# Optimization experiments

Hardware: AMD Instinct MI355X
Metric: run time of the kernel (lower is better)

The kernel has to match this reference:

```python
import jax, jax.numpy as jnp
import numpy as np

LEAK = 0.01  # torch F.leaky_relu default slope


def _conv1d(x, W, b):
    # x: [B, Cin, L], W: [Cout, Cin, K] -> [B, Cout, L-K+1]
    y = jax.lax.conv_general_dilated(x, W, window_strides=(1,), padding='VALID',
                                     dimension_numbers=('NCH', 'OIH', 'NCH'))
    return y + b[None, :, None]


def _maxpool3(x):
    # MaxPool1d(kernel=3, stride=3, padding=1); torch pads with -inf
    return jax.lax.reduce_window(x, -jnp.inf, jax.lax.max,
                                 (1, 1, 3), (1, 1, 3),
                                 ((0, 0), (0, 0), (1, 1)))


def _lrelu(x):
    return jnp.where(x >= 0, x, LEAK * x)


def _lstm_layer(x, Wih, Whh, b):
    # x: [B, T, D]; Wih: [4H, D]; Whh: [4H, H]; b: [4H]  (torch gate order i,f,g,o)
    B = x.shape[0]
    H = Whh.shape[1]

    def step(carry, xt):
        h, c = carry
        gates = xt @ Wih.T + h @ Whh.T + b  # [B, 4H]
        i, f, g, o = jnp.split(gates, 4, axis=-1)
        c = jax.nn.sigmoid(f) * c + jax.nn.sigmoid(i) * jnp.tanh(g)
        h = jax.nn.sigmoid(o) * jnp.tanh(c)
        return (h, c), h

    init = (jnp.zeros((B, H), x.dtype), jnp.zeros((B, H), x.dtype))
    _, ys = jax.lax.scan(step, init, jnp.swapaxes(x, 0, 1))
    return jnp.swapaxes(ys, 0, 1)  # [B, T, H]


def _lstm3(x, Wih_s, Whh_s, b_s):
    # 3-layer LSTM (dropout=0 in eval); return h_n[-1] + h_n[-2]
    h_last = []
    for l in range(3):
        x = _lstm_layer(x, Wih_s[l], Whh_s[l], b_s[l])
        h_last.append(x[:, -1])
    return h_last[-1] + h_last[-2]


def _forward(data_in, W1, b1, W2, b2, W3, b3,
             fWih, fWhh, fb, tWih, tWhh, tb,
             L1W, L1b, L2W, L2b, L3W, L3b, L4W, L4b):
    T, F, L, P = data_in.shape
    x = data_in.reshape(T * F, L, P).swapaxes(1, 2)  # [B, 3, L]
    x = _maxpool3(_lrelu(_conv1d(x, W1, b1)))  # [B, 10, 170]
    x = _maxpool3(_lrelu(_conv1d(x, W2, b2)))  # [B, 5, 56]
    x = _maxpool3(_lrelu(_conv1d(x, W3, b3)))  # [B, 10, 18]
    x = x.swapaxes(1, 2)                       # [B, 18, 10] packet vectors
    fv = _lstm3(x, fWih, fWhh, fb)             # [B, 10] flow vectors
    fv = fv.reshape(T, F, -1)                  # [T, F, 10]
    tv = _lstm3(fv, tWih, tWhh, tb)            # [T, 10] trace vectors
    h = _lrelu(tv @ L1W.T + L1b)
    h = _lrelu(h @ L2W.T + L2b)
    h = _lrelu(h @ L3W.T + L3b)
    return h @ L4W.T + L4b                     # [T, 7]


def setup_inputs() -> dict:
    key = jax.random.key(0)
    ks = iter(jax.random.split(key, 32))
    n = lambda shape: jax.random.normal(next(ks), shape, dtype=jnp.float32)
    return {
        'data_in': n((64, 64, 512, 3)),
        'W1': n((10, 3, 5)), 'b1': n((10,)),
        'W2': n((5, 10, 5)), 'b2': n((5,)),
        'W3': n((10, 5, 5)), 'b3': n((10,)),
        'fWih': n((3, 40, 10)), 'fWhh': n((3, 40, 10)), 'fb': n((3, 40)),
        'tWih': n((3, 40, 10)), 'tWhh': n((3, 40, 10)), 'tb': n((3, 40)),
        'L1W': n((128, 10)), 'L1b': n((128,)),
        'L2W': n((256, 128)), 'L2b': n((256,)),
        'L3W': n((64, 256)), 'L3b': n((64,)),
        'L4W': n((7, 64)), 'L4b': n((7,)),
    }


def reference(data_in, W1, b1, W2, b2, W3, b3,
              fWih, fWhh, fb, tWih, tWhh, tb,
              L1W, L1b, L2W, L2b, L3W, L3b, L4W, L4b):
    return _forward(data_in, W1, b1, W2, b2, W3, b3,
                    fWih, fWhh, fb, tWih, tWhh, tb,
                    L1W, L1b, L2W, L2b, L3W, L3b, L4W, L4b)
```

## Files before the change

### kernel.cpp

```cpp
#include <hip/hip_runtime.h>
#include <math.h>

#define LEAK 0.01f

__device__ __forceinline__ float lrelu(float x) { return fmaxf(x, LEAK * x); }
__device__ __forceinline__ float fast_rcp(float x) { return __builtin_amdgcn_rcpf(x); }
__device__ __forceinline__ float sigmoid_f(float x) {
    return fast_rcp(1.0f + exp2f(-1.44269504f * x));
}
__device__ __forceinline__ float tanh_f(float x) {
    return 2.0f * fast_rcp(1.0f + exp2f(-2.88539008f * x)) - 1.0f;
}

#define L1C 508
#define L1P 170
#define L2C 166
#define L2P 56
#define L3C 52
#define L3P 18
#define TT 18

__global__ __launch_bounds__(256) void conv_kernel(
    const float* __restrict__ in,
    const float* __restrict__ W1, const float* __restrict__ b1,
    const float* __restrict__ W2, const float* __restrict__ b2,
    const float* __restrict__ W3, const float* __restrict__ b3,
    float* __restrict__ xseq)
{
    __shared__ __align__(16) float xsraw[24 + 1536 + 24];
    __shared__ __align__(16) float y1raw[16 + L1P * 10 + 32];
    __shared__ __align__(16) float y2raw[8 + L2P * 5 + 24];
    float* xs = xsraw + 24;
    float* y1 = y1raw + 16;
    float* y2 = y2raw + 8;

    const int tid = threadIdx.x;
    const int b = blockIdx.x;

    {
        const float4* src = (const float4*)(in + (size_t)b * 1536);
        float4* dst4 = (float4*)xs;
        for (int i = tid; i < 384; i += 256) dst4[i] = src[i];
    }
    __syncthreads();

    {
        const int co = tid % 10;
        const int ob = tid / 10;
        float w[15];
        #pragma unroll
        for (int q = 0; q < 15; ++q) w[q] = W1[co * 15 + q];
        const float bias = b1[co];
        if (tid < 250) {
            for (int r = 0; r < 7; ++r) {
                int o = ob + 25 * r;
                if (o < L1P) {
                    int t0 = 3 * o - 1;
                    float a0 = bias, a1 = bias, a2 = bias;
                    #pragma unroll
                    for (int p = 0; p < 3; ++p) {
                        float yv[7];
                        #pragma unroll
                        for (int m = 0; m < 7; ++m) yv[m] = xs[3 * (t0 + m) + p];
                        #pragma unroll
                        for (int k = 0; k < 5; ++k) {
                            float wv = w[p * 5 + k];
                            a0 = fmaf(wv, yv[k], a0);
                            a1 = fmaf(wv, yv[k + 1], a1);
                            a2 = fmaf(wv, yv[k + 2], a2);
                        }
                    }
                    float best = -3.0e38f;
                    if (t0 >= 0)        best = fmaxf(best, lrelu(a0));
                    best = fmaxf(best, lrelu(a1));
                    if (t0 + 2 < L1C)   best = fmaxf(best, lrelu(a2));
                    y1[o * 10 + co] = best;
                }
            }
        }
    }
    __syncthreads();

    {
        const int co = tid % 5;
        const int ob = tid / 5;
        float w[50];
        #pragma unroll
        for (int q = 0; q < 50; ++q) w[q] = W2[co * 50 + q];
        const float bias = b2[co];
        if (tid < 255) {
            for (int r = 0; r < 2; ++r) {
                int o = ob + 51 * r;
                if (o < L2P) {
                    int t0 = 3 * o - 1;
                    float a0 = bias, a1 = bias, a2 = bias;
                    #pragma unroll
                    for (int ci = 0; ci < 10; ++ci) {
                        float yv[7];
                        #pragma unroll
                        for (int m = 0; m < 7; ++m) yv[m] = y1[(t0 + m) * 10 + ci];
                        #pragma unroll
                        for (int k = 0; k < 5; ++k) {
                            float wv = w[ci * 5 + k];
                            a0 = fmaf(wv, yv[k], a0);
                            a1 = fmaf(wv, yv[k + 1], a1);
                            a2 = fmaf(wv, yv[k + 2], a2);
                        }
                    }
                    float best = -3.0e38f;
                    if (t0 >= 0)        best = fmaxf(best, lrelu(a0));
                    best = fmaxf(best, lrelu(a1));
                    if (t0 + 2 < L2C)   best = fmaxf(best, lrelu(a2));
                    y2[o * 5 + co] = best;
                }
            }
        }
    }
    __syncthreads();

    {
        const int co = tid % 10;
        const int o = tid / 10;
        if (o < L3P) {
            float w[25];
            #pragma unroll
            for (int q = 0; q < 25; ++q) w[q] = W3[co * 25 + q];
            const float bias = b3[co];
            int t0 = 3 * o - 1;
            float a0 = bias, a1 = bias, a2 = bias;
            #pragma unroll
            for (int ci = 0; ci < 5; ++ci) {
                float yv[7];
                #pragma unroll
                for (int m = 0; m < 7; ++m) yv[m] = y2[(t0 + m) * 5 + ci];
                #pragma unroll
                for (int k = 0; k < 5; ++k) {
                    float wv = w[ci * 5 + k];
                    a0 = fmaf(wv, yv[k], a0);
                    a1 = fmaf(wv, yv[k + 1], a1);
                    a2 = fmaf(wv, yv[k + 2], a2);
                }
            }
            float best = -3.0e38f;
            if (t0 >= 0)        best = fmaxf(best, lrelu(a0));
            best = fmaxf(best, lrelu(a1));
            if (t0 + 2 < L3C)   best = fmaxf(best, lrelu(a2));
            xseq[(size_t)b * 180 + o * 10 + co] = best;
        }
    }
}

__global__ __launch_bounds__(256) void flow_lstm_kernel(
    const float* __restrict__ xseq,
    const float* __restrict__ fWih, const float* __restrict__ fWhh,
    const float* __restrict__ fb,
    float* __restrict__ fv)
{
    __shared__ __align__(16) float sbuf[3][16 * 18 * 10];
    const int tid = threadIdx.x;
    const int blk = blockIdx.x;

    {
        const float* src = xseq + (size_t)blk * 2880;
        for (int i = tid; i < 2880; i += 256) sbuf[0][i] = src[i];
    }
    __syncthreads();

    const int el = tid >> 4;
    const int j = tid & 15;
    const int jj = (j < 10) ? j : 0;
    const int base = el * 180;

    float fv_acc = 0.0f;

    for (int l = 0; l < 3; ++l) {
        const float* Wi = fWih + l * 400;
        const float* Wh = fWhh + l * 400;
        const float* bb = fb + l * 40;
        float wi0[10], wi1[10], wi2[10], wi3[10];
        float wh0[10], wh1[10], wh2[10], wh3[10];
        #pragma unroll
        for (int k = 0; k < 10; ++k) {
            wi0[k] = Wi[jj * 10 + k];
            wi1[k] = Wi[(10 + jj) * 10 + k];
            wi2[k] = Wi[(20 + jj) * 10 + k];
            wi3[k] = Wi[(30 + jj) * 10 + k];
            wh0[k] = Wh[jj * 10 + k];
            wh1[k] = Wh[(10 + jj) * 10 + k];
            wh2[k] = Wh[(20 + jj) * 10 + k];
            wh3[k] = Wh[(30 + jj) * 10 + k];
        }
        const float bi = bb[jj], bf = bb[10 + jj], bg = bb[20 + jj], bo = bb[30 + jj];

        const float* inb = sbuf[l];
        float* outb = sbuf[(l + 1) % 3];
        float c = 0.0f;
        float hj = 0.0f;

        for (int t = 0; t < TT; ++t) {
            float x[10], h[10];
            const float* xp = inb + base + t * 10;
            #pragma unroll
            for (int k = 0; k < 5; ++k) {
                float2 v = ((const float2*)xp)[k];
                x[2 * k] = v.x; x[2 * k + 1] = v.y;
            }
            if (t > 0) {
                const float* hp = outb + base + (t - 1) * 10;
                #pragma unroll
                for (int k = 0; k < 5; ++k) {
                    float2 v = ((const float2*)hp)[k];
                    h[2 * k] = v.x; h[2 * k + 1] = v.y;
                }
            } else {
                #pragma unroll
                for (int k = 0; k < 10; ++k) h[k] = 0.0f;
            }
            float gi = bi, gf = bf, gg = bg, go = bo;
            #pragma unroll
            for (int k = 0; k < 10; ++k) {
                gi = fmaf(wi0[k], x[k], gi); gi = fmaf(wh0[k], h[k], gi);
                gf = fmaf(wi1[k], x[k], gf); gf = fmaf(wh1[k], h[k], gf);
                gg = fmaf(wi2[k], x[k], gg); gg = fmaf(wh2[k], h[k], gg);
                go = fmaf(wi3[k], x[k], go); go = fmaf(wh3[k], h[k], go);
            }
            const float ai = sigmoid_f(gi), af = sigmoid_f(gf);
            const float ag = tanh_f(gg),    ao = sigmoid_f(go);
            c = af * c + ai * ag;
            hj = ao * tanh_f(c);
            if (j < 10) outb[base + t * 10 + j] = hj;
            __asm__ __volatile__("" ::: "memory");
        }
        if (l >= 1) fv_acc += hj;
    }
    if (j < 10) fv[(size_t)(blk * 16 + el) * 10 + j] = fv_acc;
}

__global__ __launch_bounds__(64) void trace_mlp_kernel(
    const float* __restrict__ fv,
    const float* __restrict__ tWih, const float* __restrict__ tWhh,
    const float* __restrict__ tb,
    const float* __restrict__ L1W, const float* __restrict__ L1b,
    const float* __restrict__ L2W, const float* __restrict__ L2b,
    const float* __restrict__ L3W, const float* __restrict__ L3b,
    const float* __restrict__ L4W, const float* __restrict__ L4b,
    float* __restrict__ out)
{
    __shared__ __align__(16) float xrow[640];
    __shared__ __align__(16) float m1[128];
    __shared__ __align__(16) float m2b[256];
    __shared__ __align__(16) float m3[64];

    const int lane = threadIdx.x;
    const int ti = blockIdx.x;

    for (int i = lane; i < 640; i += 64) xrow[i] = fv[(size_t)ti * 640 + i];
    __asm__ __volatile__("" ::: "memory");

    const int gt = lane / 10;
    const bool isg = (gt == 2);
    const float m2g = isg ? 2.0f : 1.0f;
    const float am = isg ? 2.0f : 1.0f;
    const float ab = isg ? -1.0f : 0.0f;

    const int r = (lane < 40) ? lane : 0;
    float wi0[10], wh0[10], wi1[10], wh1[10], wi2[10], wh2[10];
    #pragma unroll
    for (int k = 0; k < 10; ++k) {
        wi0[k] = tWih[r * 10 + k];
        wh0[k] = tWhh[r * 10 + k];
        wi1[k] = tWih[400 + r * 10 + k];
        wh1[k] = tWhh[400 + r * 10 + k];
        wi2[k] = tWih[800 + r * 10 + k];
        wh2[k] = tWhh[800 + r * 10 + k];
    }
    const float bs0 = tb[r], bs1 = tb[40 + r], bs2 = tb[80 + r];

    float hb0[10], hb1[10], hb2[10];
    #pragma unroll
    for (int k = 0; k < 10; ++k) { hb0[k] = 0.0f; hb1[k] = 0.0f; hb2[k] = 0.0f; }
    float c0 = 0.0f, c1 = 0.0f, c2 = 0.0f;

    for (int tick = 0; tick < 66; ++tick) {
        float xn[10];
        if (tick < 64) {
            const float* xp = xrow + tick * 10;
            #pragma unroll
            for (int k = 0; k < 5; ++k) {
                float2 v = ((const float2*)xp)[k];
                xn[2 * k] = v.x; xn[2 * k + 1] = v.y;
            }
        }
        if (tick >= 2) {
            float g = bs2;
            #pragma unroll
            for (int k = 0; k < 10; ++k) {
                g = fmaf(wi2[k], hb1[k], g);
                g = fmaf(wh2[k], hb2[k], g);
            }
            float a = am * sigmoid_f(m2g * g) + ab;
            float af = __shfl(a, lane + 10);
            float ag = __shfl(a, lane + 20);
            float ao = __shfl(a, lane + 30);
            c2 = af * c2 + a * ag;
            float h = ao * tanh_f(c2);
            #pragma unroll
            for (int k = 0; k < 10; ++k) hb2[k] = __shfl(h, k);
        }
        if (tick >= 1 && tick < 65) {
            float g = bs1;
            #pragma unroll
            for (int k = 0; k < 10; ++k) {
                g = fmaf(wi1[k], hb0[k], g);
                g = fmaf(wh1[k], hb1[k], g);
            }
            float a = am * sigmoid_f(m2g * g) + ab;
            float af = __shfl(a, lane + 10);
            float ag = __shfl(a, lane + 20);
            float ao = __shfl(a, lane + 30);
            c1 = af * c1 + a * ag;
            float h = ao * tanh_f(c1);
            #pragma unroll
            for (int k = 0; k < 10; ++k) hb1[k] = __shfl(h, k);
        }
        if (tick < 64) {
            float g = bs0;
            #pragma unroll
            for (int k = 0; k < 10; ++k) {
                g = fmaf(wi0[k], xn[k], g);
                g = fmaf(wh0[k], hb0[k], g);
            }
            float a = am * sigmoid_f(m2g * g) + ab;
            float af = __shfl(a, lane + 10);
            float ag = __shfl(a, lane + 20);
            float ao = __shfl(a, lane + 30);
            c0 = af * c0 + a * ag;
            float h = ao * tanh_f(c0);
            #pragma unroll
            for (int k = 0; k < 10; ++k) hb0[k] = __shfl(h, k);
        }
    }

    float tv[10];
    #pragma unroll
    for (int k = 0; k < 10; ++k) tv[k] = hb1[k] + hb2[k];

    {
        float a0 = L1b[lane], a1 = L1b[lane + 64];
        #pragma unroll
        for (int k = 0; k < 10; ++k) {
            a0 = fmaf(L1W[lane * 10 + k], tv[k], a0);
            a1 = fmaf(L1W[(lane + 64) * 10 + k], tv[k], a1);
        }
        m1[lane] = lrelu(a0);
        m1[lane + 64] = lrelu(a1);
    }
    __asm__ __volatile__("" ::: "memory");
    {
        float acc[4];
        #pragma unroll
        for (int q = 0; q < 4; ++q) acc[q] = L2b[lane + 64 * q];
        for (int k = 0; k < 128; ++k) {
            float hv = m1[k];
            #pragma unroll
            for (int q = 0; q < 4; ++q)
                acc[q] = fmaf(L2W[(size_t)(lane + 64 * q) * 128 + k], hv, acc[q]);
        }
        #pragma unroll
        for (int q = 0; q < 4; ++q) m2b[lane + 64 * q] = lrelu(acc[q]);
    }
    __asm__ __volatile__("" ::: "memory");
    {
        float acc = L3b[lane];
        for (int k = 0; k < 256; ++k)
            acc = fmaf(L3W[(size_t)lane * 256 + k], m2b[k], acc);
        m3[lane] = lrelu(acc);
    }
    __asm__ __volatile__("" ::: "memory");
    if (lane < 7) {
        float acc = L4b[lane];
        #pragma unroll
        for (int k = 0; k < 64; ++k)
            acc = fmaf(L4W[lane * 64 + k], m3[k], acc);
        out[ti * 7 + lane] = acc;
    }
}

extern "C" void kernel_launch(void* const* d_in, const int* in_sizes, int n_in,
                              void* d_out, int out_size, void* d_ws, size_t ws_size,
                              hipStream_t stream)
{
    const float* data_in = (const float*)d_in[0];
    const float* W1 = (const float*)d_in[1];
    const float* b1 = (const float*)d_in[2];
    const float* W2 = (const float*)d_in[3];
    const float* b2 = (const float*)d_in[4];
    const float* W3 = (const float*)d_in[5];
    const float* b3 = (const float*)d_in[6];
    const float* fWih = (const float*)d_in[7];
    const float* fWhh = (const float*)d_in[8];
    const float* fb = (const float*)d_in[9];
    const float* tWih = (const float*)d_in[10];
    const float* tWhh = (const float*)d_in[11];
    const float* tb = (const float*)d_in[12];
    const float* L1W = (const float*)d_in[13];
    const float* L1b = (const float*)d_in[14];
    const float* L2W = (const float*)d_in[15];
    const float* L2b = (const float*)d_in[16];
    const float* L3W = (const float*)d_in[17];
    const float* L3b = (const float*)d_in[18];
    const float* L4W = (const float*)d_in[19];
    const float* L4b = (const float*)d_in[20];

    float* xseq = (float*)d_ws;
    float* fv = xseq + 4096 * 180;
    float* outp = (float*)d_out;

    conv_kernel<<<4096, 256, 0, stream>>>(data_in, W1, b1, W2, b2, W3, b3, xseq);
    flow_lstm_kernel<<<256, 256, 0, stream>>>(xseq, fWih, fWhh, fb, fv);
    trace_mlp_kernel<<<64, 64, 0, stream>>>(fv, tWih, tWhh, tb,
                                            L1W, L1b, L2W, L2b, L3W, L3b,
                                            L4W, L4b, outp);
}
```

Before: 207.5 us.

## Use packed v2f math, sliding conv windows, shuffle-based LSTM hidden broadcast

Conv layer 1 now gives each thread 7 contiguous outputs and slides a register window instead of reloading inputs. Conv layers 2 and 3 use packed two-wide float vectors, and the y2 row stride is padded to 6. The flow LSTM broadcasts the hidden state with wave shuffles instead of reading it back from shared memory, prefetches the next input and uses packed dot products. The trace LSTM is peeled into explicit prologue and epilogue ticks, and the MLP tail uses float4 loads. Together these target FMA issue count and LDS traffic, at the cost of more register pressure and reordered floating-point summation.

```diff
diff --git a/kernel.cpp b/kernel.cpp
--- a/kernel.cpp
+++ b/kernel.cpp
@@ -2,6 +2,8 @@
 #include <math.h>
 
 #define LEAK 0.01f
+
+typedef float v2f __attribute__((ext_vector_type(2)));
 
 __device__ __forceinline__ float lrelu(float x) { return fmaxf(x, LEAK * x); }
 __device__ __forceinline__ float fast_rcp(float x) { return __builtin_amdgcn_rcpf(x); }
@@ -10,6 +12,15 @@
 }
 __device__ __forceinline__ float tanh_f(float x) {
     return 2.0f * fast_rcp(1.0f + exp2f(-2.88539008f * x)) - 1.0f;
+}
+
+__device__ __forceinline__ float dot10(const v2f w[5], const float h[10]) {
+    v2f acc = w[0] * (v2f){h[0], h[1]};
+    acc += w[1] * (v2f){h[2], h[3]};
+    acc += w[2] * (v2f){h[4], h[5]};
+    acc += w[3] * (v2f){h[6], h[7]};
+    acc += w[4] * (v2f){h[8], h[9]};
+    return acc.x + acc.y;
 }
 
 #define L1C 508
@@ -29,7 +40,7 @@
 {
     __shared__ __align__(16) float xsraw[24 + 1536 + 24];
     __shared__ __align__(16) float y1raw[16 + L1P * 10 + 32];
-    __shared__ __align__(16) float y2raw[8 + L2P * 5 + 24];
+    __shared__ __align__(16) float y2raw[8 + L2P * 6 + 24];
     float* xs = xsraw + 24;
     float* y1 = y1raw + 16;
     float* y2 = y2raw + 8;
@@ -47,35 +58,44 @@
     {
         const int co = tid % 10;
         const int ob = tid / 10;
-        float w[15];
-        #pragma unroll
-        for (int q = 0; q < 15; ++q) w[q] = W1[co * 15 + q];
-        const float bias = b1[co];
         if (tid < 250) {
+            float w[15];
+            #pragma unroll
+            for (int q = 0; q < 15; ++q) w[q] = W1[co * 15 + q];
+            const float bias = b1[co];
+            const int o0 = ob * 7;
+            int sb = 3 * o0 - 1;
+            float win[21];
+            #pragma unroll
+            for (int q = 0; q < 21; ++q) win[q] = xs[3 * sb + q];
+            #pragma unroll
             for (int r = 0; r < 7; ++r) {
-                int o = ob + 25 * r;
+                const int o = o0 + r;
                 if (o < L1P) {
-                    int t0 = 3 * o - 1;
                     float a0 = bias, a1 = bias, a2 = bias;
                     #pragma unroll
                     for (int p = 0; p < 3; ++p) {
-                        float yv[7];
-                        #pragma unroll
-                        for (int m = 0; m < 7; ++m) yv[m] = xs[3 * (t0 + m) + p];
                         #pragma unroll
                         for (int k = 0; k < 5; ++k) {
-                            float wv = w[p * 5 + k];
-                            a0 = fmaf(wv, yv[k], a0);
-                            a1 = fmaf(wv, yv[k + 1], a1);
-                            a2 = fmaf(wv, yv[k + 2], a2);
+                            const float wv = w[p * 5 + k];
+                            a0 = fmaf(wv, win[3 * k + p], a0);
+                            a1 = fmaf(wv, win[3 * (k + 1) + p], a1);
+                            a2 = fmaf(wv, win[3 * (k + 2) + p], a2);
                         }
                     }
                     float best = -3.0e38f;
-                    if (t0 >= 0)        best = fmaxf(best, lrelu(a0));
+                    if (sb >= 0)        best = fmaxf(best, lrelu(a0));
                     best = fmaxf(best, lrelu(a1));
-                    if (t0 + 2 < L1C)   best = fmaxf(best, lrelu(a2));
+                    if (sb + 2 < L1C)   best = fmaxf(best, lrelu(a2));
                     y1[o * 10 + co] = best;
                 }
+                if (r < 6 && o + 1 < L1P) {
+                    #pragma unroll
+                    for (int q = 0; q < 12; ++q) win[q] = win[q + 9];
+                    #pragma unroll
+                    for (int q = 0; q < 9; ++q) win[12 + q] = xs[3 * sb + 21 + q];
+                    sb += 3;
+                }
             }
         }
     }
@@ -84,34 +104,45 @@
     {
         const int co = tid % 5;
         const int ob = tid / 5;
-        float w[50];
-        #pragma unroll
-        for (int q = 0; q < 50; ++q) w[q] = W2[co * 50 + q];
+        v2f wv2[25];
+        #pragma unroll
+        for (int c2 = 0; c2 < 5; ++c2)
+            #pragma unroll
+            for (int k = 0; k < 5; ++k)
+                wv2[c2 * 5 + k] = (v2f){W2[co * 50 + (2 * c2) * 5 + k],
+                                        W2[co * 50 + (2 * c2 + 1) * 5 + k]};
         const float bias = b2[co];
         if (tid < 255) {
             for (int r = 0; r < 2; ++r) {
-                int o = ob + 51 * r;
+                const int o = ob + 51 * r;
                 if (o < L2P) {
-                    int t0 = 3 * o - 1;
-                    float a0 = bias, a1 = bias, a2 = bias;
+                    const int t0 = 3 * o - 1;
+                    v2f rows[7][5];
                     #pragma unroll
-                    for (int ci = 0; ci < 10; ++ci) {
-                        float yv[7];
+                    for (int m = 0; m < 7; ++m) {
+                        const v2f* pr = (const v2f*)(y1 + (t0 + m) * 10);
                         #pragma unroll
-                        for (int m = 0; m < 7; ++m) yv[m] = y1[(t0 + m) * 10 + ci];
+                        for (int c2 = 0; c2 < 5; ++c2) rows[m][c2] = pr[c2];
+                    }
+                    v2f v0 = {0.f, 0.f}, v1 = {0.f, 0.f}, v2 = {0.f, 0.f};
+                    #pragma unroll
+                    for (int c2 = 0; c2 < 5; ++c2) {
                         #pragma unroll
                         for (int k = 0; k < 5; ++k) {
-                            float wv = w[ci * 5 + k];
-                            a0 = fmaf(wv, yv[k], a0);
-                            a1 = fmaf(wv, yv[k + 1], a1);
-                            a2 = fmaf(wv, yv[k + 2], a2);
+                            const v2f wv = wv2[c2 * 5 + k];
+                            v0 += wv * rows[k][c2];
+                            v1 += wv * rows[k + 1][c2];
+                            v2 += wv * rows[k + 2][c2];
                         }
                     }
+                    const float a0 = bias + v0.x + v0.y;
+                    const float a1 = bias + v1.x + v1.y;
+                    const float a2 = bias + v2.x + v2.y;
                     float best = -3.0e38f;
                     if (t0 >= 0)        best = fmaxf(best, lrelu(a0));
                     best = fmaxf(best, lrelu(a1));
                     if (t0 + 2 < L2C)   best = fmaxf(best, lrelu(a2));
-                    y2[o * 5 + co] = best;
+                    y2[o * 6 + co] = best;
                 }
             }
         }
@@ -122,25 +153,48 @@
         const int co = tid % 10;
         const int o = tid / 10;
         if (o < L3P) {
-            float w[25];
-            #pragma unroll
-            for (int q = 0; q < 25; ++q) w[q] = W3[co * 25 + q];
+            v2f wv3[10];
+            float ws3[5];
+            #pragma unroll
+            for (int c2 = 0; c2 < 2; ++c2)
+                #pragma unroll
+                for (int k = 0; k < 5; ++k)
+                    wv3[c2 * 5 + k] = (v2f){W3[co * 25 + (2 * c2) * 5 + k],
+                                            W3[co * 25 + (2 * c2 + 1) * 5 + k]};
+            #pragma unroll
+            for (int k = 0; k < 5; ++k) ws3[k] = W3[co * 25 + 20 + k];
             const float bias = b3[co];
-            int t0 = 3 * o - 1;
-            float a0 = bias, a1 = bias, a2 = bias;
-            #pragma unroll
-            for (int ci = 0; ci < 5; ++ci) {
-                float yv[7];
-                #pragma unroll
-                for (int m = 0; m < 7; ++m) yv[m] = y2[(t0 + m) * 5 + ci];
+            const int t0 = 3 * o - 1;
+            v2f ra[7][2];
+            float rc[7];
+            #pragma unroll
+            for (int m = 0; m < 7; ++m) {
+                const float* base = y2 + (t0 + m) * 6;
+                ra[m][0] = ((const v2f*)base)[0];
+                ra[m][1] = ((const v2f*)base)[1];
+                rc[m] = base[4];
+            }
+            v2f v0 = {0.f, 0.f}, v1 = {0.f, 0.f}, v2 = {0.f, 0.f};
+            float s0 = 0.f, s1 = 0.f, s2 = 0.f;
+            #pragma unroll
+            for (int c2 = 0; c2 < 2; ++c2) {
                 #pragma unroll
                 for (int k = 0; k < 5; ++k) {
-                    float wv = w[ci * 5 + k];
-                    a0 = fmaf(wv, yv[k], a0);
-                    a1 = fmaf(wv, yv[k + 1], a1);
-                    a2 = fmaf(wv, yv[k + 2], a2);
+                    const v2f wv = wv3[c2 * 5 + k];
+                    v0 += wv * ra[k][c2];
+                    v1 += wv * ra[k + 1][c2];
+                    v2 += wv * ra[k + 2][c2];
                 }
             }
+            #pragma unroll
+            for (int k = 0; k < 5; ++k) {
+                s0 = fmaf(ws3[k], rc[k], s0);
+                s1 = fmaf(ws3[k], rc[k + 1], s1);
+                s2 = fmaf(ws3[k], rc[k + 2], s2);
+            }
+            const float a0 = bias + s0 + v0.x + v0.y;
+            const float a1 = bias + s1 + v1.x + v1.y;
+            const float a2 = bias + s2 + v2.x + v2.y;
             float best = -3.0e38f;
             if (t0 >= 0)        best = fmaxf(best, lrelu(a0));
             best = fmaxf(best, lrelu(a1));
@@ -170,6 +224,8 @@
     const int j = tid & 15;
     const int jj = (j < 10) ? j : 0;
     const int base = el * 180;
+    const int lane = tid & 63;
+    const int gbase = lane & 48;
 
     float fv_acc = 0.0f;
 
@@ -177,61 +233,54 @@
         const float* Wi = fWih + l * 400;
         const float* Wh = fWhh + l * 400;
         const float* bb = fb + l * 40;
-        float wi0[10], wi1[10], wi2[10], wi3[10];
-        float wh0[10], wh1[10], wh2[10], wh3[10];
-        #pragma unroll
-        for (int k = 0; k < 10; ++k) {
-            wi0[k] = Wi[jj * 10 + k];
-            wi1[k] = Wi[(10 + jj) * 10 + k];
-            wi2[k] = Wi[(20 + jj) * 10 + k];
-            wi3[k] = Wi[(30 + jj) * 10 + k];
-            wh0[k] = Wh[jj * 10 + k];
-            wh1[k] = Wh[(10 + jj) * 10 + k];
-            wh2[k] = Wh[(20 + jj) * 10 + k];
-            wh3[k] = Wh[(30 + jj) * 10 + k];
+        v2f wi0[5], wi1[5], wi2[5], wi3[5], wh0[5], wh1[5], wh2[5], wh3[5];
+        #pragma unroll
+        for (int k = 0; k < 5; ++k) {
+            wi0[k] = ((const v2f*)(Wi + jj * 10))[k];
+            wi1[k] = ((const v2f*)(Wi + (10 + jj) * 10))[k];
+            wi2[k] = ((const v2f*)(Wi + (20 + jj) * 10))[k];
+            wi3[k] = ((const v2f*)(Wi + (30 + jj) * 10))[k];
+            wh0[k] = ((const v2f*)(Wh + jj * 10))[k];
+            wh1[k] = ((const v2f*)(Wh + (10 + jj) * 10))[k];
+            wh2[k] = ((const v2f*)(Wh + (20 + jj) * 10))[k];
+            wh3[k] = ((const v2f*)(Wh + (30 + jj) * 10))[k];
         }
         const float bi = bb[jj], bf = bb[10 + jj], bg = bb[20 + jj], bo = bb[30 + jj];
 
         const float* inb = sbuf[l];
         float* outb = sbuf[(l + 1) % 3];
-        float c = 0.0f;
-        float hj = 0.0f;
+        float c = 0.0f, hj = 0.0f;
+        float h[10], xc[10], xn[10];
+        #pragma unroll
+        for (int k = 0; k < 10; ++k) h[k] = 0.0f;
+        {
+            const v2f* p = (const v2f*)(inb + base);
+            #pragma unroll
+            for (int k = 0; k < 5; ++k) { v2f v = p[k]; xc[2*k] = v.x; xc[2*k+1] = v.y; }
+        }
 
         for (int t = 0; t < TT; ++t) {
-            float x[10], h[10];
-            const float* xp = inb + base + t * 10;
-            #pragma unroll
-            for (int k = 0; k < 5; ++k) {
-                float2 v = ((const float2*)xp)[k];
-                x[2 * k] = v.x; x[2 * k + 1] = v.y;
-            }
-            if (t > 0) {
-                const float* hp = outb + base + (t - 1) * 10;
+            if (t + 1 < TT) {
+                const v2f* p = (const v2f*)(inb + base + (t + 1) * 10);
                 #pragma unroll
-                for (int k = 0; k < 5; ++k) {
-                    float2 v = ((const float2*)hp)[k];
-                    h[2 * k] = v.x; h[2 * k + 1] = v.y;
-                }
-            } else {
-                #pragma unroll
-                for (int k = 0; k < 10; ++k) h[k] = 0.0f;
-            }
-            float gi = bi, gf = bf, gg = bg, go = bo;
-            #pragma unroll
-            for (int k = 0; k < 10; ++k) {
-                gi = fmaf(wi0[k], x[k], gi); gi = fmaf(wh0[k], h[k], gi);
-                gf = fmaf(wi1[k], x[k], gf); gf = fmaf(wh1[k], h[k], gf);
-                gg = fmaf(wi2[k], x[k], gg); gg = fmaf(wh2[k], h[k], gg);
-                go = fmaf(wi3[k], x[k], go); go = fmaf(wh3[k], h[k], go);
-            }
+                for (int k = 0; k < 5; ++k) { v2f v = p[k]; xn[2*k] = v.x; xn[2*k+1] = v.y; }
+            }
+            float gi = bi + dot10(wi0, xc) + dot10(wh0, h);
+            float gf = bf + dot10(wi1, xc) + dot10(wh1, h);
+            float gg = bg + dot10(wi2, xc) + dot10(wh2, h);
+            float go = bo + dot10(wi3, xc) + dot10(wh3, h);
             const float ai = sigmoid_f(gi), af = sigmoid_f(gf);
             const float ag = tanh_f(gg),    ao = sigmoid_f(go);
             c = af * c + ai * ag;
             hj = ao * tanh_f(c);
             if (j < 10) outb[base + t * 10 + j] = hj;
-            __asm__ __volatile__("" ::: "memory");
+            #pragma unroll
+            for (int k = 0; k < 10; ++k) h[k] = __shfl(hj, gbase + k);
+            #pragma unroll
+            for (int k = 0; k < 10; ++k) xc[k] = xn[k];
         }
         if (l >= 1) fv_acc += hj;
+        __asm__ __volatile__("" ::: "memory");
     }
     if (j < 10) fv[(size_t)(blk * 16 + el) * 10 + j] = fv_acc;
 }
@@ -254,7 +303,11 @@
     const int lane = threadIdx.x;
     const int ti = blockIdx.x;
 
-    for (int i = lane; i < 640; i += 64) xrow[i] = fv[(size_t)ti * 640 + i];
+    {
+        const float4* src = (const float4*)(fv + (size_t)ti * 640);
+        float4* dst = (float4*)xrow;
+        for (int i = lane; i < 160; i += 64) dst[i] = src[i];
+    }
     __asm__ __volatile__("" ::: "memory");
 
     const int gt = lane / 10;
@@ -264,15 +317,15 @@
     const float ab = isg ? -1.0f : 0.0f;
 
     const int r = (lane < 40) ? lane : 0;
-    float wi0[10], wh0[10], wi1[10], wh1[10], wi2[10], wh2[10];
+    v2f wi0[5], wh0[5], wi1[5], wh1[5], wi2[5], wh2[5];
     #pragma unroll
-    for (int k = 0; k < 10; ++k) {
-        wi0[k] = tWih[r * 10 + k];
-        wh0[k] = tWhh[r * 10 + k];
-        wi1[k] = tWih[400 + r * 10 + k];
-        wh1[k] = tWhh[400 + r * 10 + k];
-        wi2[k] = tWih[800 + r * 10 + k];
-        wh2[k] = tWhh[800 + r * 10 + k];
+    for (int k = 0; k < 5; ++k) {
+        wi0[k] = ((const v2f*)(tWih + r * 10))[k];
+        wh0[k] = ((const v2f*)(tWhh + r * 10))[k];
+        wi1[k] = ((const v2f*)(tWih + 400 + r * 10))[k];
+        wh1[k] = ((const v2f*)(tWhh + 400 + r * 10))[k];
+        wi2[k] = ((const v2f*)(tWih + 800 + r * 10))[k];
+        wh2[k] = ((const v2f*)(tWhh + 800 + r * 10))[k];
     }
     const float bs0 = tb[r], bs1 = tb[40 + r], bs2 = tb[80 + r];
 
@@ -281,77 +334,64 @@
     for (int k = 0; k < 10; ++k) { hb0[k] = 0.0f; hb1[k] = 0.0f; hb2[k] = 0.0f; }
     float c0 = 0.0f, c1 = 0.0f, c2 = 0.0f;
 
-    for (int tick = 0; tick < 66; ++tick) {
-        float xn[10];
-        if (tick < 64) {
-            const float* xp = xrow + tick * 10;
-            #pragma unroll
-            for (int k = 0; k < 5; ++k) {
-                float2 v = ((const float2*)xp)[k];
-                xn[2 * k] = v.x; xn[2 * k + 1] = v.y;
-            }
-        }
-        if (tick >= 2) {
-            float g = bs2;
-            #pragma unroll
-            for (int k = 0; k < 10; ++k) {
-                g = fmaf(wi2[k], hb1[k], g);
-                g = fmaf(wh2[k], hb2[k], g);
-            }
-            float a = am * sigmoid_f(m2g * g) + ab;
-            float af = __shfl(a, lane + 10);
-            float ag = __shfl(a, lane + 20);
-            float ao = __shfl(a, lane + 30);
-            c2 = af * c2 + a * ag;
-            float h = ao * tanh_f(c2);
-            #pragma unroll
-            for (int k = 0; k < 10; ++k) hb2[k] = __shfl(h, k);
-        }
-        if (tick >= 1 && tick < 65) {
-            float g = bs1;
-            #pragma unroll
-            for (int k = 0; k < 10; ++k) {
-                g = fmaf(wi1[k], hb0[k], g);
-                g = fmaf(wh1[k], hb1[k], g);
-            }
-            float a = am * sigmoid_f(m2g * g) + ab;
-            float af = __shfl(a, lane + 10);
-            float ag = __shfl(a, lane + 20);
-            float ao = __shfl(a, lane + 30);
-            c1 = af * c1 + a * ag;
-            float h = ao * tanh_f(c1);
-            #pragma unroll
-            for (int k = 0; k < 10; ++k) hb1[k] = __shfl(h, k);
-        }
-        if (tick < 64) {
-            float g = bs0;
-            #pragma unroll
-            for (int k = 0; k < 10; ++k) {
-                g = fmaf(wi0[k], xn[k], g);
-                g = fmaf(wh0[k], hb0[k], g);
-            }
-            float a = am * sigmoid_f(m2g * g) + ab;
-            float af = __shfl(a, lane + 10);
-            float ag = __shfl(a, lane + 20);
-            float ao = __shfl(a, lane + 30);
-            c0 = af * c0 + a * ag;
-            float h = ao * tanh_f(c0);
-            #pragma unroll
-            for (int k = 0; k < 10; ++k) hb0[k] = __shfl(h, k);
-        }
-    }
+    float xc[10], xn[10];
+    auto loadx = [&](float* d, int t) __attribute__((always_inline)) {
+        const v2f* p = (const v2f*)(xrow + t * 10);
+        #pragma unroll
+        for (int k = 0; k < 5; ++k) { v2f v = p[k]; d[2*k] = v.x; d[2*k+1] = v.y; }
+    };
+    auto cpx = [&]() __attribute__((always_inline)) {
+        #pragma unroll
+        for (int k = 0; k < 10; ++k) xc[k] = xn[k];
+    };
+    auto tick = [&](bool D0, bool D1, bool D2) __attribute__((always_inline)) {
+        float g0f = 0.f, g1f = 0.f, g2f = 0.f;
+        if (D2) g2f = bs2 + dot10(wi2, hb1) + dot10(wh2, hb2);
+        if (D1) g1f = bs1 + dot10(wi1, hb0) + dot10(wh1, hb1);
+        if (D0) g0f = bs0 + dot10(wi0, xc) + dot10(wh0, hb0);
+        float a0 = 0.f, a1 = 0.f, a2 = 0.f;
+        if (D2) a2 = am * sigmoid_f(m2g * g2f) + ab;
+        if (D1) a1 = am * sigmoid_f(m2g * g1f) + ab;
+        if (D0) a0 = am * sigmoid_f(m2g * g0f) + ab;
+        float f2, q2, o2, f1, q1, o1, f0, q0, o0;
+        if (D2) { f2 = __shfl(a2, lane + 10); q2 = __shfl(a2, lane + 20); o2 = __shfl(a2, lane + 30); }
+        if (D1) { f1 = __shfl(a1, lane + 10); q1 = __shfl(a1, lane + 20); o1 = __shfl(a1, lane + 30); }
+        if (D0) { f0 = __shfl(a0, lane + 10); q0 = __shfl(a0, lane + 20); o0 = __shfl(a0, lane + 30); }
+        float h2 = 0.f, h1 = 0.f, h0 = 0.f;
+        if (D2) { c2 = f2 * c2 + a2 * q2; h2 = o2 * tanh_f(c2); }
+        if (D1) { c1 = f1 * c1 + a1 * q1; h1 = o1 * tanh_f(c1); }
+        if (D0) { c0 = f0 * c0 + a0 * q0; h0 = o0 * tanh_f(c0); }
+        #pragma unroll
+        for (int k = 0; k < 10; ++k) {
+            if (D2) hb2[k] = __shfl(h2, k);
+            if (D1) hb1[k] = __shfl(h1, k);
+            if (D0) hb0[k] = __shfl(h0, k);
+        }
+    };
+
+    loadx(xc, 0);
+    loadx(xn, 1);
+    tick(true, false, false); cpx();
+    loadx(xn, 2);
+    tick(true, true, false); cpx();
+    for (int tau = 2; tau < 63; ++tau) {
+        loadx(xn, tau + 1);
+        tick(true, true, true);
+        cpx();
+    }
+    tick(true, true, true);
+    tick(false, true, true);
+    tick(false, false, true);
 
     float tv[10];
     #pragma unroll
     for (int k = 0; k < 10; ++k) tv[k] = hb1[k] + hb2[k];
 
     {
-        float a0 = L1b[lane], a1 = L1b[lane + 64];
-        #pragma unroll
-        for (int k = 0; k < 10; ++k) {
-            a0 = fmaf(L1W[lane * 10 + k], tv[k], a0);
-            a1 = fmaf(L1W[(lane + 64) * 10 + k], tv[k], a1);
-        }
+        const v2f* w0 = (const v2f*)(L1W + lane * 10);
+        const v2f* w1 = (const v2f*)(L1W + (lane + 64) * 10);
+        float a0 = L1b[lane] + dot10(w0, tv);
+        float a1 = L1b[lane + 64] + dot10(w1, tv);
         m1[lane] = lrelu(a0);
         m1[lane + 64] = lrelu(a1);
     }
@@ -360,11 +400,16 @@
         float acc[4];
         #pragma unroll
         for (int q = 0; q < 4; ++q) acc[q] = L2b[lane + 64 * q];
-        for (int k = 0; k < 128; ++k) {
-            float hv = m1[k];
-            #pragma unroll
-            for (int q = 0; q < 4; ++q)
-                acc[q] = fmaf(L2W[(size_t)(lane + 64 * q) * 128 + k], hv, acc[q]);
+        for (int k = 0; k < 128; k += 4) {
+            float4 hv = *(const float4*)(m1 + k);
+            #pragma unroll
+            for (int q = 0; q < 4; ++q) {
+                float4 wv = *(const float4*)(L2W + (size_t)(lane + 64 * q) * 128 + k);
+                acc[q] = fmaf(wv.x, hv.x, acc[q]);
+                acc[q] = fmaf(wv.y, hv.y, acc[q]);
+                acc[q] = fmaf(wv.z, hv.z, acc[q]);
+                acc[q] = fmaf(wv.w, hv.w, acc[q]);
+            }
         }
         #pragma unroll
         for (int q = 0; q < 4; ++q) m2b[lane + 64 * q] = lrelu(acc[q]);
@@ -372,16 +417,28 @@
     __asm__ __volatile__("" ::: "memory");
     {
         float acc = L3b[lane];
-        for (int k = 0; k < 256; ++k)
-            acc = fmaf(L3W[(size_t)lane * 256 + k], m2b[k], acc);
+        for (int k = 0; k < 256; k += 4) {
+            float4 hv = *(const float4*)(m2b + k);
+            float4 wv = *(const float4*)(L3W + (size_t)lane * 256 + k);
+            acc = fmaf(wv.x, hv.x, acc);
+            acc = fmaf(wv.y, hv.y, acc);
+            acc = fmaf(wv.z, hv.z, acc);
+            acc = fmaf(wv.w, hv.w, acc);
+        }
         m3[lane] = lrelu(acc);
     }
     __asm__ __volatile__("" ::: "memory");
     if (lane < 7) {
         float acc = L4b[lane];
         #pragma unroll
-        for (int k = 0; k < 64; ++k)
-            acc = fmaf(L4W[lane * 64 + k], m3[k], acc);
+        for (int k = 0; k < 64; k += 4) {
+            float4 hv = *(const float4*)(m3 + k);
+            float4 wv = *(const float4*)(L4W + lane * 64 + k);
+            acc = fmaf(wv.x, hv.x, acc);
+            acc = fmaf(wv.y, hv.y, acc);
+            acc = fmaf(wv.z, hv.z, acc);
+            acc = fmaf(wv.w, hv.w, acc);
+        }
         out[ti * 7 + lane] = acc;
     }
 }
```

New measurement: 207.5 us. Within noise of the previous version (+0.0%).
